# Kernel optimization log

Measured on AMD Instinct MI355X. Metric: run time of the kernel, lower is better.

The kernel has to match this reference:

```python
import jax, jax.numpy as jnp
import numpy as np

B, S, D, H = 32, 512, 256, 512  # batch, seq_len, input_dim, hidden_dim (512 hardcoded in source)


def setup_inputs() -> dict:
    key = jax.random.key(0)
    ks = jax.random.split(key, 24)
    sc = 1.0 / np.sqrt(H)

    def p(k, shape):
        return (jax.random.normal(k, shape, jnp.float32) * sc).astype(jnp.float32)

    return {
        "x": jax.random.normal(ks[0], (B, S, D), jnp.float32),
        # encoder forward direction (PyTorch LSTM gate order i,f,g,o)
        "Wih_f": p(ks[1], (4 * H, D)), "Whh_f": p(ks[2], (4 * H, H)), "b_f": p(ks[3], (4 * H,)),
        # encoder reverse direction
        "Wih_r": p(ks[4], (4 * H, D)), "Whh_r": p(ks[5], (4 * H, H)), "b_r": p(ks[6], (4 * H,)),
        # decoder LSTM (input never used: decoder_input is always zeros in the source)
        "Wih_d": p(ks[7], (4 * H, H)), "Whh_d": p(ks[8], (4 * H, H)), "b_d": p(ks[9], (4 * H,)),
        # reduce_h / reduce_c
        "Wr_h": p(ks[10], (H, 2 * H)), "br_h": p(ks[11], (H,)),
        "Wr_c": p(ks[12], (H, 2 * H)), "br_c": p(ks[13], (H,)),
        # pointer attention
        "W1": p(ks[14], (H, H)), "b1": p(ks[15], (H,)),
        "W2": p(ks[16], (H, H)), "b2": p(ks[17], (H,)),
        "vt": p(ks[18], (1, H)), "bvt": p(ks[19], (1,)),
    }


def _lstm_cell(h, c, z):
    i, f, g, o = jnp.split(z, 4, axis=-1)
    c_new = jax.nn.sigmoid(f) * c + jax.nn.sigmoid(i) * jnp.tanh(g)
    h_new = jax.nn.sigmoid(o) * jnp.tanh(c_new)
    return h_new, c_new


def _run_lstm(xs, Wih, Whh, b):
    """xs: [S, B, D] -> (outputs [S,B,H], h_T [B,H], c_T [B,H])"""
    Bn = xs.shape[1]
    Hn = Whh.shape[1]
    init = (jnp.zeros((Bn, Hn), xs.dtype), jnp.zeros((Bn, Hn), xs.dtype))
    x_proj = jnp.einsum('sbd,gd->sbg', xs, Wih) + b  # precompute input contribution

    def step(carry, xp):
        h, c = carry
        h, c = _lstm_cell(h, c, xp + h @ Whh.T)
        return (h, c), h

    (hT, cT), hs = jax.lax.scan(step, init, x_proj)
    return hs, hT, cT


def reference(x, Wih_f, Whh_f, b_f, Wih_r, Whh_r, b_r,
              Wih_d, Whh_d, b_d, Wr_h, br_h, Wr_c, br_c,
              W1, b1, W2, b2, vt, bvt):
    xs = jnp.swapaxes(x, 0, 1)  # [S, B, D]
    hs_f, hf, cf = _run_lstm(xs, Wih_f, Whh_f, b_f)
    hs_r, hr, cr = _run_lstm(xs[::-1], Wih_r, Whh_r, b_r)
    hs_r = hs_r[::-1]

    h_d = jnp.concatenate([hf, hr], axis=-1) @ Wr_h.T + br_h  # [B, H]
    c_d = jnp.concatenate([cf, cr], axis=-1) @ Wr_c.T + br_c

    enc_red = hs_f + hs_r  # [S, B, H]  (enc_out[...,:512] + enc_out[...,512:])
    pre1 = jnp.einsum('sbh,kh->sbk', enc_red, W1) + b1  # W1(enc) precomputed once

    seq_len = x.shape[1]

    def dec_step(carry, _):
        h, c = carry
        # decoder_input is always zeros -> Wih_d contribution is exactly 0
        h, c = _lstm_cell(h, c, h @ Whh_d.T + b_d)
        att = jnp.tanh(pre1 + (h @ W2.T + b2)[None])      # [S, B, H]
        scores = jnp.einsum('sbh,h->sb', att, vt[0]) + bvt[0]
        return (h, c), scores.T  # [B, S]

    _, logits = jax.lax.scan(dec_step, (h_d, c_d), None, length=seq_len)
    return jnp.swapaxes(logits, 0, 1)  # [B, seq_len, S]
```

## Files before the change

### kernel.cpp

```cpp
#include <hip/hip_runtime.h>
#include <hip/hip_bf16.h>
#include <cstdint>
#include <cstddef>

#define B_ 32
#define S_ 512
#define D_ 256
#define H_ 512

typedef _Float16 h2 __attribute__((ext_vector_type(2)));
typedef _Float16 h4 __attribute__((ext_vector_type(4)));
typedef _Float16 h8 __attribute__((ext_vector_type(8)));
typedef float f32x4 __attribute__((ext_vector_type(4)));
typedef unsigned u32x4 __attribute__((ext_vector_type(4)));

__device__ __forceinline__ h2 H2(unsigned u) { return __builtin_bit_cast(h2, u); }
__device__ __forceinline__ unsigned U2(h2 v) { return __builtin_bit_cast(unsigned, v); }

#if __has_builtin(__builtin_amdgcn_exp2f)
__device__ __forceinline__ float exp2_fast(float x) { return __builtin_amdgcn_exp2f(x); }
#else
__device__ __forceinline__ float exp2_fast(float x) { return exp2f(x); }
#endif
#if __has_builtin(__builtin_amdgcn_rcpf)
__device__ __forceinline__ float rcp_fast(float x) { return __builtin_amdgcn_rcpf(x); }
#else
__device__ __forceinline__ float rcp_fast(float x) { return 1.0f / x; }
#endif

__device__ __forceinline__ float sigm(float x) {
  return rcp_fast(1.0f + exp2_fast(-1.4426950408889634f * x));
}
__device__ __forceinline__ float tanh_fast(float x) {
  return 1.0f - 2.0f * rcp_fast(1.0f + exp2_fast(2.8853900817779268f * x));
}

__device__ __forceinline__ uint4 coh_load16(const void* p) {
  u32x4 v;
  asm volatile("global_load_dwordx4 %0, %1, off sc0 sc1"
               : "=v"(v) : "v"(p) : "memory");
  return __builtin_bit_cast(uint4, v);
}
__device__ __forceinline__ void vm_drain() {
  asm volatile("s_waitcnt vmcnt(0)" ::: "memory");
}

__device__ __forceinline__ bool valid16(uint4 v) {
  return ((v.x & 0xFFFFu) != 0xFFFFu) && ((v.x >> 16) != 0xFFFFu) &&
         ((v.y & 0xFFFFu) != 0xFFFFu) && ((v.y >> 16) != 0xFFFFu) &&
         ((v.z & 0xFFFFu) != 0xFFFFu) && ((v.z >> 16) != 0xFFFFu) &&
         ((v.w & 0xFFFFu) != 0xFFFFu) && ((v.w >> 16) != 0xFFFFu);
}

__device__ __forceinline__ void h_store(unsigned short* p, unsigned short v) {
  __hip_atomic_store(p, v, __ATOMIC_RELAXED, __HIP_MEMORY_SCOPE_AGENT);
}

__global__ __launch_bounds__(256) void fill_sent_k(uint4* __restrict__ dst, size_t n16) {
  uint4 s = {0xFFFFFFFFu, 0xFFFFFFFFu, 0xFFFFFFFFu, 0xFFFFFFFFu};
  size_t stride = (size_t)gridDim.x * 256;
  for (size_t i = (size_t)blockIdx.x * 256 + threadIdx.x; i < n16; i += stride)
    dst[i] = s;
}

__global__ __launch_bounds__(256) void f2h_k(const float* __restrict__ src,
                                             _Float16* __restrict__ dst, int n4) {
  int i = blockIdx.x * 256 + threadIdx.x;
  if (i < n4) {
    float4 v = ((const float4*)src)[i];
    h4 o = {(_Float16)v.x, (_Float16)v.y, (_Float16)v.z, (_Float16)v.w};
    ((h4*)dst)[i] = o;
  }
}

__global__ __launch_bounds__(256, 1) void enc_coop_k(
    const _Float16* __restrict__ xh,
    const _Float16* __restrict__ WihF, const _Float16* __restrict__ WhhF, const float* __restrict__ bF,
    const _Float16* __restrict__ WihR, const _Float16* __restrict__ WhhR, const float* __restrict__ bR,
    float* __restrict__ cF, float* __restrict__ cR,
    _Float16* __restrict__ hsF, _Float16* __restrict__ hsR)
{
  __shared__ __align__(16) _Float16 cbuf[96][16][8];
  __shared__ float zfin[4][16][17];
  __shared__ float cls[16][17];

  const int bid = blockIdx.x;
  const int group = bid >> 5;
  const int dir = group >> 1;
  const int bh0 = (group & 1) << 4;
  const int jb = bid & 31;
  const int c0 = jb << 4;
  const int tid = threadIdx.x;
  const int lane = tid & 63;
  const int wv = tid >> 6;

  const _Float16* __restrict__ Wih = dir ? WihR : WihF;
  const _Float16* __restrict__ Whh = dir ? WhhR : WhhF;
  const float* __restrict__ bias = dir ? bR : bF;
  _Float16* __restrict__ hs = dir ? hsR : hsF;
  float* __restrict__ cOut = dir ? cR : cF;

  h8 aw[24];
  {
    const int m = lane & 15, kg = lane >> 4;
    const int wrow = wv * H_ + c0 + m;
    const _Float16* wi = Wih + (size_t)wrow * D_;
    const _Float16* wh = Whh + (size_t)wrow * H_;
    #pragma unroll
    for (int tu = 0; tu < 24; ++tu) {
      int k = tu * 32 + kg * 8;
      aw[tu] = (k < 256) ? *(const h8*)(wi + k) : *(const h8*)(wh + (k - 256));
    }
  }

  const int cc = tid & 15, cb = tid >> 4;
  float bvg[4];
  #pragma unroll
  for (int g = 0; g < 4; ++g) bvg[g] = bias[g * H_ + c0 + cc];

  const char* cbase = (const char*)cbuf + (size_t)((lane >> 4) * 256 + (lane & 15) * 16);
  const int sn = tid & 15;
  const int xo = (tid >> 4) * 2;
  const int ho = (tid >> 4) * 4;
  __syncthreads();

  for (int t = 0; t < S_; ++t) {
    const int xi = dir ? (S_ - 1 - t) : t;

    {
      const _Float16* xp = xh + ((size_t)(bh0 + sn) * S_ + xi) * D_;
      uint4 v0 = *(const uint4*)(xp + xo * 8);
      uint4 v1 = *(const uint4*)(xp + xo * 8 + 8);
      *(uint4*)&cbuf[xo][sn][0] = v0;
      *(uint4*)&cbuf[xo + 1][sn][0] = v1;
    }
    __syncthreads();

    f32x4 acc = {0.f, 0.f, 0.f, 0.f};
    #pragma unroll
    for (int tu = 0; tu < 8; ++tu) {
      h8 bf = *(const h8*)(cbase + tu * 1024);
      acc = __builtin_amdgcn_mfma_f32_16x16x32_f16(aw[tu], bf, acc, 0, 0, 0);
    }

    {
      if (t == 0) {
        uint4 z = {0, 0, 0, 0};
        #pragma unroll
        for (int u = 0; u < 4; ++u) *(uint4*)&cbuf[32 + ho + u][sn][0] = z;
      } else {
        const int xip = dir ? xi + 1 : xi - 1;
        const _Float16* hbase = hs + ((size_t)xip * B_ + bh0 + sn) * H_;
        uint4 vs[4];
        unsigned pend = 0xF;
        do {
          #pragma unroll
          for (int u = 0; u < 4; ++u)
            if (pend & (1u << u)) vs[u] = coh_load16(hbase + (ho + u) * 8);
          vm_drain();
          #pragma unroll
          for (int u = 0; u < 4; ++u)
            if ((pend & (1u << u)) && valid16(vs[u])) pend &= ~(1u << u);
        } while (pend);
        #pragma unroll
        for (int u = 0; u < 4; ++u) *(uint4*)&cbuf[32 + ho + u][sn][0] = vs[u];
      }
    }
    __syncthreads();

    #pragma unroll
    for (int tu = 8; tu < 24; ++tu) {
      h8 bf = *(const h8*)(cbase + tu * 1024);
      acc = __builtin_amdgcn_mfma_f32_16x16x32_f16(aw[tu], bf, acc, 0, 0, 0);
    }
    {
      const int mrow = (lane >> 4) * 4, n = lane & 15;
      #pragma unroll
      for (int r = 0; r < 4; ++r) zfin[wv][mrow + r][n] = acc[r];
    }
    __syncthreads();

    {
      const float zi = zfin[0][cc][cb] + bvg[0];
      const float zf = zfin[1][cc][cb] + bvg[1];
      const float zg = zfin[2][cc][cb] + bvg[2];
      const float zo = zfin[3][cc][cb] + bvg[3];
      const float c_old = (t == 0) ? 0.f : cls[cc][cb];
      const float cn = sigm(zf) * c_old + sigm(zi) * tanh_fast(zg);
      const float hn = sigm(zo) * tanh_fast(cn);
      cls[cc][cb] = cn;
      _Float16 hh = (_Float16)hn;
      h_store((unsigned short*)(hs + ((size_t)xi * B_ + bh0 + cb) * H_ + c0 + cc),
              __builtin_bit_cast(unsigned short, hh));
      if (t == S_ - 1) cOut[(size_t)(bh0 + cb) * H_ + c0 + cc] = cn;
    }
    __syncthreads();
  }
}

__global__ __launch_bounds__(256, 1) void dec_coop_k(
    const float* __restrict__ hd0, const float* __restrict__ cD0,
    const _Float16* __restrict__ Whh, const float* __restrict__ bias,
    _Float16* __restrict__ hdec)
{
  __shared__ __align__(16) _Float16 cbuf[64][16][8];
  __shared__ float zfin[4][16][17];
  __shared__ float cls[16][17];

  const int bid = blockIdx.x;
  const int group = bid >> 5;
  const int bh0 = group << 4;
  const int jb = bid & 31;
  const int c0 = jb << 4;
  const int tid = threadIdx.x;
  const int lane = tid & 63;
  const int wv = tid >> 6;

  h8 aw[16];
  {
    const int m = lane & 15, kg = lane >> 4;
    const _Float16* wh = Whh + (size_t)(wv * H_ + c0 + m) * H_;
    #pragma unroll
    for (int tu = 0; tu < 16; ++tu) aw[tu] = *(const h8*)(wh + tu * 32 + kg * 8);
  }

  const int cc = tid & 15, cb = tid >> 4;
  float bvg[4];
  #pragma unroll
  for (int g = 0; g < 4; ++g) bvg[g] = bias[g * H_ + c0 + cc];
  cls[cc][cb] = cD0[(size_t)(bh0 + cb) * H_ + c0 + cc];

  const char* cbase = (const char*)cbuf + (size_t)((lane >> 4) * 256 + (lane & 15) * 16);
  const int sn = tid & 15, ho = (tid >> 4) * 4;
  __syncthreads();

  for (int t = 0; t < S_; ++t) {
    {
      if (t == 0) {
        const float* src = hd0 + (size_t)(bh0 + sn) * H_;
        #pragma unroll
        for (int u = 0; u < 4; ++u) {
          float4 f0 = *(const float4*)(src + (ho + u) * 8);
          float4 f1 = *(const float4*)(src + (ho + u) * 8 + 4);
          h8 o = {(_Float16)f0.x, (_Float16)f0.y, (_Float16)f0.z, (_Float16)f0.w,
                  (_Float16)f1.x, (_Float16)f1.y, (_Float16)f1.z, (_Float16)f1.w};
          *(h8*)&cbuf[ho + u][sn][0] = o;
        }
      } else {
        const _Float16* src = hdec + ((size_t)(t - 1) * B_ + bh0 + sn) * H_;
        uint4 vs[4];
        unsigned pend = 0xF;
        do {
          #pragma unroll
          for (int u = 0; u < 4; ++u)
            if (pend & (1u << u)) vs[u] = coh_load16(src + (ho + u) * 8);
          vm_drain();
          #pragma unroll
          for (int u = 0; u < 4; ++u)
            if ((pend & (1u << u)) && valid16(vs[u])) pend &= ~(1u << u);
        } while (pend);
        #pragma unroll
        for (int u = 0; u < 4; ++u) *(uint4*)&cbuf[ho + u][sn][0] = vs[u];
      }
    }
    __syncthreads();

    f32x4 acc = {0.f, 0.f, 0.f, 0.f};
    #pragma unroll
    for (int tu = 0; tu < 16; ++tu) {
      h8 bf = *(const h8*)(cbase + tu * 1024);
      acc = __builtin_amdgcn_mfma_f32_16x16x32_f16(aw[tu], bf, acc, 0, 0, 0);
    }
    {
      const int mrow = (lane >> 4) * 4, n = lane & 15;
      #pragma unroll
      for (int r = 0; r < 4; ++r) zfin[wv][mrow + r][n] = acc[r];
    }
    __syncthreads();

    {
      const float zi = zfin[0][cc][cb] + bvg[0];
      const float zf = zfin[1][cc][cb] + bvg[1];
      const float zg = zfin[2][cc][cb] + bvg[2];
      const float zo = zfin[3][cc][cb] + bvg[3];
      const float cn = sigm(zf) * cls[cc][cb] + sigm(zi) * tanh_fast(zg);
      const float hn = sigm(zo) * tanh_fast(cn);
      cls[cc][cb] = cn;
      _Float16 hh = (_Float16)hn;
      h_store((unsigned short*)(hdec + ((size_t)t * B_ + bh0 + cb) * H_ + c0 + cc),
              __builtin_bit_cast(unsigned short, hh));
    }
    __syncthreads();
  }
}

template <int MODE>
__global__ __launch_bounds__(256) void gemm_mfma_k(
    const _Float16* __restrict__ A1, const _Float16* __restrict__ A2,
    const _Float16* __restrict__ W, const float* __restrict__ bias,
    _Float16* __restrict__ C)
{
  __shared__ __align__(16) _Float16 Abuf[4][66][8];
  __shared__ __align__(16) _Float16 Bbuf[4][66][8];
  const int tid = threadIdx.x;
  const int m0 = blockIdx.x * 64, n0 = blockIdx.y * 64;
  const int lane = tid & 63, wv = tid >> 6;
  const int sr = tid >> 2, sk = tid & 3;
  f32x4 acc[4] = {{0.f,0.f,0.f,0.f},{0.f,0.f,0.f,0.f},
                  {0.f,0.f,0.f,0.f},{0.f,0.f,0.f,0.f}};

  for (int kc = 0; kc < H_; kc += 32) {
    __syncthreads();
    {
      uint4 a = *(const uint4*)(A1 + (size_t)(m0 + sr) * H_ + kc + sk * 8);
      if (MODE == 1) {
        uint4 a2 = *(const uint4*)(A2 + (size_t)(m0 + sr) * H_ + kc + sk * 8);
        a.x = U2(H2(a.x) + H2(a2.x)); a.y = U2(H2(a.y) + H2(a2.y));
        a.z = U2(H2(a.z) + H2(a2.z)); a.w = U2(H2(a.w) + H2(a2.w));
      }
      *(uint4*)&Abuf[sk][sr][0] = a;
      uint4 b = *(const uint4*)(W + (size_t)(n0 + sr) * H_ + kc + sk * 8);
      *(uint4*)&Bbuf[sk][sr][0] = b;
    }
    __syncthreads();
    const int fr = lane & 15, kg = lane >> 4;
    h8 af = *(const h8*)&Abuf[kg][wv * 16 + fr][0];
    #pragma unroll
    for (int nt = 0; nt < 4; ++nt) {
      h8 bf = *(const h8*)&Bbuf[kg][nt * 16 + fr][0];
      acc[nt] = __builtin_amdgcn_mfma_f32_16x16x32_f16(af, bf, acc[nt], 0, 0, 0);
    }
  }
  const int fr = lane & 15, fq = lane >> 4;
  #pragma unroll
  for (int nt = 0; nt < 4; ++nt) {
    const int n = n0 + nt * 16 + fr;
    const float bv = bias[n];
    #pragma unroll
    for (int r = 0; r < 4; ++r) {
      const int m = m0 + wv * 16 + fq * 4 + r;
      C[(size_t)m * H_ + n] = (_Float16)(acc[nt][r] + bv);
    }
  }
}

__device__ __forceinline__ float4 load4f(const float* p) { return *(const float4*)p; }
__device__ __forceinline__ float4 load4f(const _Float16* p) {
  uint2 u = *(const uint2*)p;
  h2 a = H2(u.x), b = H2(u.y);
  return make_float4((float)a.x, (float)a.y, (float)b.x, (float)b.y);
}

template <typename T>
__global__ __launch_bounds__(256) void gemm_cat_small_k(
    const T* __restrict__ A1, const T* __restrict__ A2,
    const float* __restrict__ W, const float* __restrict__ bias,
    float* __restrict__ C)
{
  const int tid = threadIdx.x;
  const int col = tid & 31;
  const int rg  = tid >> 5;
  const int n   = blockIdx.y * 32 + col;
  float acc[4] = {0, 0, 0, 0};
  #pragma unroll
  for (int pass = 0; pass < 2; ++pass) {
    const T* __restrict__ A = pass ? A2 : A1;
    const float4* __restrict__ w4 = (const float4*)(W + (size_t)n * 1024 + pass * 512);
    for (int k4 = 0; k4 < 128; ++k4) {
      float4 w = w4[k4];
      #pragma unroll
      for (int i = 0; i < 4; ++i) {
        int row = rg + (i << 3);
        float4 a = load4f(A + (size_t)row * H_ + k4 * 4);
        acc[i] += w.x * a.x + w.y * a.y + w.z * a.z + w.w * a.w;
      }
    }
  }
  const float bv = bias[n];
  #pragma unroll
  for (int i = 0; i < 4; ++i) {
    int row = rg + (i << 3);
    C[(size_t)row * H_ + n] = acc[i] + bv;
  }
}

__global__ __launch_bounds__(256) void sumv_k(const float* __restrict__ vt,
                                              float* __restrict__ o) {
  __shared__ float sh[4];
  float v = vt[threadIdx.x] + vt[threadIdx.x + 256];
  #pragma unroll
  for (int d = 32; d; d >>= 1) v += __shfl_down(v, d, 64);
  if ((threadIdx.x & 63) == 0) sh[threadIdx.x >> 6] = v;
  __syncthreads();
  if (threadIdx.x == 0) o[0] = sh[0] + sh[1] + sh[2] + sh[3];
}

#define KT_ 2.8853900817779268f
__global__ __launch_bounds__(256) void attn_k(
    const _Float16* __restrict__ pre1, const _Float16* __restrict__ Qm,
    const float* __restrict__ vt, const float* __restrict__ bvt,
    const float* __restrict__ sumv, float* __restrict__ out)
{
  __shared__ float sp[16][260];
  __shared__ float sq[16][260];
  __shared__ float sv[256];
  const int b = blockIdx.z, tbase = blockIdx.y << 4, sbase = blockIdx.x << 4;
  const int tid = threadIdx.x;
  const int so = tid & 15, to = tid >> 4;
  float acc0 = 0.f, acc1 = 0.f;
  const float cfin = sumv[0] + bvt[0];

  for (int h0 = 0; h0 < H_; h0 += 256) {
    __syncthreads();
    {
      const int i = tid & 15, hoo = (tid >> 4) * 16;
      const _Float16* qp = Qm + ((size_t)(tbase + i) * B_ + b) * H_ + h0 + hoo;
      const _Float16* pp = pre1 + ((size_t)(sbase + i) * B_ + b) * H_ + h0 + hoo;
      h8 q0 = *(const h8*)qp, q1 = *(const h8*)(qp + 8);
      h8 p0 = *(const h8*)pp, p1 = *(const h8*)(pp + 8);
      #pragma unroll
      for (int j = 0; j < 8; ++j) {
        sq[i][hoo + j]     = exp2_fast(fminf(fmaxf(KT_ * (float)q0[j], -60.f), 60.f));
        sq[i][hoo + 8 + j] = exp2_fast(fminf(fmaxf(KT_ * (float)q1[j], -60.f), 60.f));
        sp[i][hoo + j]     = exp2_fast(fminf(fmaxf(KT_ * (float)p0[j], -60.f), 60.f));
        sp[i][hoo + 8 + j] = exp2_fast(fminf(fmaxf(KT_ * (float)p1[j], -60.f), 60.f));
      }
    }
    sv[tid] = vt[h0 + tid];
    __syncthreads();
    #pragma unroll 8
    for (int h4_ = 0; h4_ < 64; ++h4_) {
      float4 p = *(const float4*)&sp[so][h4_ * 4];
      float4 q = *(const float4*)&sq[to][h4_ * 4];
      float4 vv = *(const float4*)&sv[h4_ * 4];
      acc0 = fmaf(vv.x, rcp_fast(fmaf(p.x, q.x, 1.0f)), acc0);
      acc1 = fmaf(vv.y, rcp_fast(fmaf(p.y, q.y, 1.0f)), acc1);
      acc0 = fmaf(vv.z, rcp_fast(fmaf(p.z, q.z, 1.0f)), acc0);
      acc1 = fmaf(vv.w, rcp_fast(fmaf(p.w, q.w, 1.0f)), acc1);
    }
  }
  out[((size_t)b * S_ + tbase + to) * S_ + sbase + so] = cfin - 2.f * (acc0 + acc1);
}

extern "C" void kernel_launch(void* const* d_in, const int* in_sizes, int n_in,
                              void* d_out, int out_size, void* d_ws, size_t ws_size,
                              hipStream_t stream)
{
  (void)in_sizes; (void)n_in; (void)out_size; (void)ws_size;
  const float* x     = (const float*)d_in[0];
  const float* WihF  = (const float*)d_in[1];
  const float* WhhF  = (const float*)d_in[2];
  const float* bF    = (const float*)d_in[3];
  const float* WihR  = (const float*)d_in[4];
  const float* WhhR  = (const float*)d_in[5];
  const float* bR    = (const float*)d_in[6];
  const float* WhhD  = (const float*)d_in[8];
  const float* bD    = (const float*)d_in[9];
  const float* Wr_h  = (const float*)d_in[10];
  const float* br_h  = (const float*)d_in[11];
  const float* Wr_c  = (const float*)d_in[12];
  const float* br_c  = (const float*)d_in[13];
  const float* W1    = (const float*)d_in[14];
  const float* b1    = (const float*)d_in[15];
  const float* W2    = (const float*)d_in[16];
  const float* b2    = (const float*)d_in[17];
  const float* vt    = (const float*)d_in[18];
  const float* bvt   = (const float*)d_in[19];
  float* out = (float*)d_out;

  const size_t SBH = (size_t)S_ * B_ * H_;
  const size_t BH  = (size_t)B_ * H_;

  _Float16* hp = (_Float16*)d_ws;
  _Float16* hs_f  = hp;              hp += SBH;
  _Float16* hs_r  = hp;              hp += SBH;
  _Float16* hdec  = hp;              hp += SBH;
  _Float16* pre1h = hp;              hp += SBH;
  _Float16* Qmh   = hp;              hp += SBH;
  _Float16* xh    = hp;              hp += (size_t)B_ * S_ * D_;
  _Float16* wihF  = hp;              hp += (size_t)4 * H_ * D_;
  _Float16* wihR  = hp;              hp += (size_t)4 * H_ * D_;
  _Float16* whhF  = hp;              hp += (size_t)4 * H_ * H_;
  _Float16* whhR  = hp;              hp += (size_t)4 * H_ * H_;
  _Float16* whhD  = hp;              hp += (size_t)4 * H_ * H_;
  _Float16* w1h   = hp;              hp += (size_t)H_ * H_;
  _Float16* w2h   = hp;              hp += (size_t)H_ * H_;
  float* fp  = (float*)hp;
  float* cF  = fp;                   fp += BH;
  float* cR  = fp;                   fp += BH;
  float* cD  = fp;                   fp += BH;
  float* hd0 = fp;                   fp += BH;
  float* sumv = fp;

  fill_sent_k<<<2048, 256, 0, stream>>>((uint4*)hs_f, 3 * SBH / 8);

  f2h_k<<<(B_ * S_ * D_ / 4 + 255) / 256, 256, 0, stream>>>(x, xh, B_ * S_ * D_ / 4);
  f2h_k<<<(4 * H_ * D_ / 4 + 255) / 256, 256, 0, stream>>>(WihF, wihF, 4 * H_ * D_ / 4);
  f2h_k<<<(4 * H_ * D_ / 4 + 255) / 256, 256, 0, stream>>>(WihR, wihR, 4 * H_ * D_ / 4);
  f2h_k<<<(4 * H_ * H_ / 4 + 255) / 256, 256, 0, stream>>>(WhhF, whhF, 4 * H_ * H_ / 4);
  f2h_k<<<(4 * H_ * H_ / 4 + 255) / 256, 256, 0, stream>>>(WhhR, whhR, 4 * H_ * H_ / 4);
  f2h_k<<<(4 * H_ * H_ / 4 + 255) / 256, 256, 0, stream>>>(WhhD, whhD, 4 * H_ * H_ / 4);
  f2h_k<<<(H_ * H_ / 4 + 255) / 256, 256, 0, stream>>>(W1, w1h, H_ * H_ / 4);
  f2h_k<<<(H_ * H_ / 4 + 255) / 256, 256, 0, stream>>>(W2, w2h, H_ * H_ / 4);
  sumv_k<<<1, 256, 0, stream>>>(vt, sumv);

  enc_coop_k<<<128, 256, 0, stream>>>(xh, wihF, whhF, bF, wihR, whhR, bR,
                                      cF, cR, hs_f, hs_r);

  gemm_cat_small_k<_Float16><<<dim3(1, 16), 256, 0, stream>>>(
      hs_f + (size_t)(S_ - 1) * BH, hs_r, Wr_h, br_h, hd0);
  gemm_cat_small_k<float><<<dim3(1, 16), 256, 0, stream>>>(cF, cR, Wr_c, br_c, cD);

  gemm_mfma_k<1><<<dim3(256, 8), 256, 0, stream>>>(hs_f, hs_r, w1h, b1, pre1h);

  dec_coop_k<<<64, 256, 0, stream>>>(hd0, cD, whhD, bD, hdec);

  gemm_mfma_k<0><<<dim3(256, 8), 256, 0, stream>>>(hdec, nullptr, w2h, b2, Qmh);

  attn_k<<<dim3(32, 32, 32), 256, 0, stream>>>(pre1h, Qmh, vt, bvt, sumv, out);
}
```

Before: 3.374 ms.

## Fuse prep kernels, split MFMA accumulators, drop trailing per-step barriers

```diff
diff --git a/kernel.cpp b/kernel.cpp
--- a/kernel.cpp
+++ b/kernel.cpp
@@ -56,20 +56,47 @@
   __hip_atomic_store(p, v, __ATOMIC_RELAXED, __HIP_MEMORY_SCOPE_AGENT);
 }
 
-__global__ __launch_bounds__(256) void fill_sent_k(uint4* __restrict__ dst, size_t n16) {
-  uint4 s = {0xFFFFFFFFu, 0xFFFFFFFFu, 0xFFFFFFFFu, 0xFFFFFFFFu};
-  size_t stride = (size_t)gridDim.x * 256;
-  for (size_t i = (size_t)blockIdx.x * 256 + threadIdx.x; i < n16; i += stride)
-    dst[i] = s;
-}
-
-__global__ __launch_bounds__(256) void f2h_k(const float* __restrict__ src,
-                                             _Float16* __restrict__ dst, int n4) {
-  int i = blockIdx.x * 256 + threadIdx.x;
-  if (i < n4) {
-    float4 v = ((const float4*)src)[i];
+#define N_X   1048576u
+#define N_WIH 131072u
+#define N_WHH 262144u
+#define N_W1  65536u
+#define C0_ N_X
+#define C1_ (C0_ + N_WIH)
+#define C2_ (C1_ + N_WIH)
+#define C3_ (C2_ + N_WHH)
+#define C4_ (C3_ + N_WHH)
+#define C5_ (C4_ + N_WHH)
+#define C6_ (C5_ + N_W1)
+#define NCV (C6_ + N_W1)
+__global__ __launch_bounds__(256) void prep_k(
+    const float* __restrict__ x,
+    const float* __restrict__ WihF, const float* __restrict__ WihR,
+    const float* __restrict__ WhhF, const float* __restrict__ WhhR,
+    const float* __restrict__ WhhD,
+    const float* __restrict__ W1, const float* __restrict__ W2,
+    _Float16* __restrict__ xh, _Float16* __restrict__ wihF, _Float16* __restrict__ wihR,
+    _Float16* __restrict__ whhF, _Float16* __restrict__ whhR, _Float16* __restrict__ whhD,
+    _Float16* __restrict__ w1h, _Float16* __restrict__ w2h,
+    uint4* __restrict__ sent)
+{
+  const size_t stride = (size_t)gridDim.x * 256;
+  const size_t NS = 3ull * S_ * B_ * H_ / 8;
+  uint4 sv = {0xFFFFFFFFu, 0xFFFFFFFFu, 0xFFFFFFFFu, 0xFFFFFFFFu};
+  for (size_t j = (size_t)blockIdx.x * 256 + threadIdx.x; j < NS; j += stride)
+    sent[j] = sv;
+  for (size_t j = (size_t)blockIdx.x * 256 + threadIdx.x; j < NCV; j += stride) {
+    const float* src; _Float16* dst; size_t off;
+    if (j < C0_)      { src = x;    dst = xh;   off = j; }
+    else if (j < C1_) { src = WihF; dst = wihF; off = j - C0_; }
+    else if (j < C2_) { src = WihR; dst = wihR; off = j - C1_; }
+    else if (j < C3_) { src = WhhF; dst = whhF; off = j - C2_; }
+    else if (j < C4_) { src = WhhR; dst = whhR; off = j - C3_; }
+    else if (j < C5_) { src = WhhD; dst = whhD; off = j - C4_; }
+    else if (j < C6_) { src = W1;   dst = w1h;  off = j - C5_; }
+    else              { src = W2;   dst = w2h;  off = j - C6_; }
+    float4 v = ((const float4*)src)[off];
     h4 o = {(_Float16)v.x, (_Float16)v.y, (_Float16)v.z, (_Float16)v.w};
-    ((h4*)dst)[i] = o;
+    ((h4*)dst)[off] = o;
   }
 }
 
@@ -136,11 +163,13 @@
     }
     __syncthreads();
 
-    f32x4 acc = {0.f, 0.f, 0.f, 0.f};
-    #pragma unroll
-    for (int tu = 0; tu < 8; ++tu) {
-      h8 bf = *(const h8*)(cbase + tu * 1024);
-      acc = __builtin_amdgcn_mfma_f32_16x16x32_f16(aw[tu], bf, acc, 0, 0, 0);
+    f32x4 acc0 = {0.f, 0.f, 0.f, 0.f}, acc1 = {0.f, 0.f, 0.f, 0.f};
+    #pragma unroll
+    for (int tu = 0; tu < 8; tu += 2) {
+      h8 b0 = *(const h8*)(cbase + tu * 1024);
+      h8 b1 = *(const h8*)(cbase + (tu + 1) * 1024);
+      acc0 = __builtin_amdgcn_mfma_f32_16x16x32_f16(aw[tu], b0, acc0, 0, 0, 0);
+      acc1 = __builtin_amdgcn_mfma_f32_16x16x32_f16(aw[tu + 1], b1, acc1, 0, 0, 0);
     }
 
     {
@@ -169,14 +198,16 @@
     __syncthreads();
 
     #pragma unroll
-    for (int tu = 8; tu < 24; ++tu) {
-      h8 bf = *(const h8*)(cbase + tu * 1024);
-      acc = __builtin_amdgcn_mfma_f32_16x16x32_f16(aw[tu], bf, acc, 0, 0, 0);
+    for (int tu = 8; tu < 24; tu += 2) {
+      h8 b0 = *(const h8*)(cbase + tu * 1024);
+      h8 b1 = *(const h8*)(cbase + (tu + 1) * 1024);
+      acc0 = __builtin_amdgcn_mfma_f32_16x16x32_f16(aw[tu], b0, acc0, 0, 0, 0);
+      acc1 = __builtin_amdgcn_mfma_f32_16x16x32_f16(aw[tu + 1], b1, acc1, 0, 0, 0);
     }
     {
       const int mrow = (lane >> 4) * 4, n = lane & 15;
       #pragma unroll
-      for (int r = 0; r < 4; ++r) zfin[wv][mrow + r][n] = acc[r];
+      for (int r = 0; r < 4; ++r) zfin[wv][mrow + r][n] = acc0[r] + acc1[r];
     }
     __syncthreads();
 
@@ -194,7 +225,6 @@
               __builtin_bit_cast(unsigned short, hh));
       if (t == S_ - 1) cOut[(size_t)(bh0 + cb) * H_ + c0 + cc] = cn;
     }
-    __syncthreads();
   }
 }
 
@@ -265,16 +295,18 @@
     }
     __syncthreads();
 
-    f32x4 acc = {0.f, 0.f, 0.f, 0.f};
-    #pragma unroll
-    for (int tu = 0; tu < 16; ++tu) {
-      h8 bf = *(const h8*)(cbase + tu * 1024);
-      acc = __builtin_amdgcn_mfma_f32_16x16x32_f16(aw[tu], bf, acc, 0, 0, 0);
+    f32x4 acc0 = {0.f, 0.f, 0.f, 0.f}, acc1 = {0.f, 0.f, 0.f, 0.f};
+    #pragma unroll
+    for (int tu = 0; tu < 16; tu += 2) {
+      h8 b0 = *(const h8*)(cbase + tu * 1024);
+      h8 b1 = *(const h8*)(cbase + (tu + 1) * 1024);
+      acc0 = __builtin_amdgcn_mfma_f32_16x16x32_f16(aw[tu], b0, acc0, 0, 0, 0);
+      acc1 = __builtin_amdgcn_mfma_f32_16x16x32_f16(aw[tu + 1], b1, acc1, 0, 0, 0);
     }
     {
       const int mrow = (lane >> 4) * 4, n = lane & 15;
       #pragma unroll
-      for (int r = 0; r < 4; ++r) zfin[wv][mrow + r][n] = acc[r];
+      for (int r = 0; r < 4; ++r) zfin[wv][mrow + r][n] = acc0[r] + acc1[r];
     }
     __syncthreads();
 
@@ -290,7 +322,6 @@
       h_store((unsigned short*)(hdec + ((size_t)t * B_ + bh0 + cb) * H_ + c0 + cc),
               __builtin_bit_cast(unsigned short, hh));
     }
-    __syncthreads();
   }
 }
 
@@ -351,28 +382,46 @@
   return make_float4((float)a.x, (float)a.y, (float)b.x, (float)b.y);
 }
 
-template <typename T>
-__global__ __launch_bounds__(256) void gemm_cat_small_k(
-    const T* __restrict__ A1, const T* __restrict__ A2,
-    const float* __restrict__ W, const float* __restrict__ bias,
-    float* __restrict__ C)
+__global__ __launch_bounds__(256) void dec_init_k(
+    const _Float16* __restrict__ hfl, const _Float16* __restrict__ hr,
+    const float* __restrict__ cF, const float* __restrict__ cR,
+    const float* __restrict__ Wr_h, const float* __restrict__ br_h,
+    const float* __restrict__ Wr_c, const float* __restrict__ br_c,
+    float* __restrict__ hd0, float* __restrict__ cD)
 {
   const int tid = threadIdx.x;
   const int col = tid & 31;
   const int rg  = tid >> 5;
-  const int n   = blockIdx.y * 32 + col;
+  const int which = (int)blockIdx.y >> 4;
+  const int n = ((int)blockIdx.y & 15) * 32 + col;
+  const float* W = which ? Wr_c : Wr_h;
+  const float* bias = which ? br_c : br_h;
+  float* C = which ? cD : hd0;
   float acc[4] = {0, 0, 0, 0};
   #pragma unroll
   for (int pass = 0; pass < 2; ++pass) {
-    const T* __restrict__ A = pass ? A2 : A1;
     const float4* __restrict__ w4 = (const float4*)(W + (size_t)n * 1024 + pass * 512);
-    for (int k4 = 0; k4 < 128; ++k4) {
-      float4 w = w4[k4];
-      #pragma unroll
-      for (int i = 0; i < 4; ++i) {
-        int row = rg + (i << 3);
-        float4 a = load4f(A + (size_t)row * H_ + k4 * 4);
-        acc[i] += w.x * a.x + w.y * a.y + w.z * a.z + w.w * a.w;
+    if (which) {
+      const float* A = pass ? cR : cF;
+      for (int k4 = 0; k4 < 128; ++k4) {
+        float4 w = w4[k4];
+        #pragma unroll
+        for (int i = 0; i < 4; ++i) {
+          int row = rg + (i << 3);
+          float4 a = load4f(A + (size_t)row * H_ + k4 * 4);
+          acc[i] += w.x * a.x + w.y * a.y + w.z * a.z + w.w * a.w;
+        }
+      }
+    } else {
+      const _Float16* A = pass ? hr : hfl;
+      for (int k4 = 0; k4 < 128; ++k4) {
+        float4 w = w4[k4];
+        #pragma unroll
+        for (int i = 0; i < 4; ++i) {
+          int row = rg + (i << 3);
+          float4 a = load4f(A + (size_t)row * H_ + k4 * 4);
+          acc[i] += w.x * a.x + w.y * a.y + w.z * a.z + w.w * a.w;
+        }
       }
     }
   }
@@ -492,24 +541,17 @@
   float* hd0 = fp;                   fp += BH;
   float* sumv = fp;
 
-  fill_sent_k<<<2048, 256, 0, stream>>>((uint4*)hs_f, 3 * SBH / 8);
-
-  f2h_k<<<(B_ * S_ * D_ / 4 + 255) / 256, 256, 0, stream>>>(x, xh, B_ * S_ * D_ / 4);
-  f2h_k<<<(4 * H_ * D_ / 4 + 255) / 256, 256, 0, stream>>>(WihF, wihF, 4 * H_ * D_ / 4);
-  f2h_k<<<(4 * H_ * D_ / 4 + 255) / 256, 256, 0, stream>>>(WihR, wihR, 4 * H_ * D_ / 4);
-  f2h_k<<<(4 * H_ * H_ / 4 + 255) / 256, 256, 0, stream>>>(WhhF, whhF, 4 * H_ * H_ / 4);
-  f2h_k<<<(4 * H_ * H_ / 4 + 255) / 256, 256, 0, stream>>>(WhhR, whhR, 4 * H_ * H_ / 4);
-  f2h_k<<<(4 * H_ * H_ / 4 + 255) / 256, 256, 0, stream>>>(WhhD, whhD, 4 * H_ * H_ / 4);
-  f2h_k<<<(H_ * H_ / 4 + 255) / 256, 256, 0, stream>>>(W1, w1h, H_ * H_ / 4);
-  f2h_k<<<(H_ * H_ / 4 + 255) / 256, 256, 0, stream>>>(W2, w2h, H_ * H_ / 4);
+  prep_k<<<2048, 256, 0, stream>>>(x, WihF, WihR, WhhF, WhhR, WhhD, W1, W2,
+                                   xh, wihF, wihR, whhF, whhR, whhD, w1h, w2h,
+                                   (uint4*)hs_f);
   sumv_k<<<1, 256, 0, stream>>>(vt, sumv);
 
   enc_coop_k<<<128, 256, 0, stream>>>(xh, wihF, whhF, bF, wihR, whhR, bR,
                                       cF, cR, hs_f, hs_r);
 
-  gemm_cat_small_k<_Float16><<<dim3(1, 16), 256, 0, stream>>>(
-      hs_f + (size_t)(S_ - 1) * BH, hs_r, Wr_h, br_h, hd0);
-  gemm_cat_small_k<float><<<dim3(1, 16), 256, 0, stream>>>(cF, cR, Wr_c, br_c, cD);
+  dec_init_k<<<dim3(1, 32), 256, 0, stream>>>(
+      hs_f + (size_t)(S_ - 1) * BH, hs_r, cF, cR,
+      Wr_h, br_h, Wr_c, br_c, hd0, cD);
 
   gemm_mfma_k<1><<<dim3(256, 8), 256, 0, stream>>>(hs_f, hs_r, w1h, b1, pre1h);
 
```

New measurement: 3.331 ms. Within noise of the previous version (-1.3%).
